# Optimization experiments

Hardware: AMD Instinct MI355X
Metric: run time of the kernel (lower is better)

Reference implementation:

```python
import jax, jax.numpy as jnp
import numpy as np

B, S = 16, 32768
LEVELS = (5, 20)
TIME_DIM = 8
NUM_FREQS = 6  # frequency xyz encoder: 3*(1+2*6)=39 dims
HID = 128
IN_DIM = 3 * (1 + 2 * NUM_FREQS) + 2 * TIME_DIM  # 55


def setup_inputs() -> dict:
    key = jax.random.key(0)
    ks = jax.random.split(key, 16)
    time = jax.random.uniform(ks[0], (B,), dtype=jnp.float32)
    xyz = jax.random.uniform(ks[1], (B, S, 3), dtype=jnp.float32) * 2.0 - 1.0  # in [-1,1]
    te0 = jax.random.normal(ks[2], (LEVELS[0] + 1, TIME_DIM), dtype=jnp.float32)
    te1 = jax.random.normal(ks[3], (LEVELS[1] + 1, TIME_DIM), dtype=jnp.float32)
    W0 = jax.random.normal(ks[4], (IN_DIM, HID), dtype=jnp.float32) * 0.05
    b0 = jnp.zeros((HID,), dtype=jnp.float32)
    W1 = jax.random.normal(ks[5], (HID, HID), dtype=jnp.float32) * 0.05
    b1 = jnp.zeros((HID,), dtype=jnp.float32)
    W2 = jax.random.normal(ks[6], (HID, HID), dtype=jnp.float32) * 0.05
    b2 = jnp.zeros((HID,), dtype=jnp.float32)
    Wout = jax.random.normal(ks[7], (HID, 1), dtype=jnp.float32) * 0.05
    bout = jnp.zeros((1,), dtype=jnp.float32)
    return {"time": time, "xyz": xyz, "te0": te0, "te1": te1,
            "W0": W0, "b0": b0, "W1": W1, "b1": b1, "W2": W2, "b2": b2,
            "Wout": Wout, "bout": bout}


def _time_encode(t, emb, L):
    # bucketize t into L uniform intervals on [0,1), lerp between bucket endpoints
    tL = t * L
    idx = jnp.clip(jnp.floor(tL).astype(jnp.int32), 0, L - 1)  # (B,)
    w = (idx + 1).astype(t.dtype) - tL                          # weight for lower endpoint
    lerped = w[:, None] * emb[idx] + (1.0 - w)[:, None] * emb[idx + 1]
    # t >= 1: use last embedding directly (torch fallback branch)
    return jnp.where((t >= 1.0)[:, None], emb[L][None, :], lerped)


def _xyz_encode(x):
    # frequency encoding, include_input, freqs 2^0..2^(NUM_FREQS-1)
    freqs = jnp.asarray(2.0 ** np.arange(NUM_FREQS), dtype=x.dtype)  # (F,)
    xp = x[:, None, :] * freqs[None, :, None]                         # (N, F, 3)
    n = x.shape[0]
    return jnp.concatenate([x, jnp.sin(xp).reshape(n, -1), jnp.cos(xp).reshape(n, -1)], axis=-1)


def reference(time, xyz, te0, te1, W0, b0, W1, b1, W2, b2, Wout, bout):
    s = xyz.shape[1]
    t_enc = jnp.concatenate([_time_encode(time, te0, LEVELS[0]),
                             _time_encode(time, te1, LEVELS[1])], axis=-1)  # (B, 16)
    t_enc = jnp.repeat(t_enc, s, axis=0)          # (B*S, 16)  'B d -> (B S) d'
    pts = (xyz.reshape(-1, 3) + 1.0) / 2.0        # (B*S, 3)
    x = jnp.concatenate([t_enc, _xyz_encode(pts)], axis=1)  # (B*S, 55)
    x = jax.nn.relu(x @ W0 + b0)
    x = jax.nn.relu(x @ W1 + b1)
    x = jax.nn.relu(x @ W2 + b2)
    return x @ Wout + bout  # (B*S, 1)
```

## Files before the change

kernel.cpp:

```cpp
#include <hip/hip_runtime.h>

typedef _Float16 f16;
typedef __attribute__((ext_vector_type(2))) __fp16 fp16x2;
typedef __attribute__((ext_vector_type(8))) _Float16 f16x8;
typedef __attribute__((ext_vector_type(4))) float f32x4;
typedef __attribute__((ext_vector_type(4))) unsigned int u32x4;

#define NPTS   (16 * 32768)
#define W0P_OFF 0
#define W1P_OFF (16 * 1024)
#define W2P_OFF (48 * 1024)
#define WOP_OFF (80 * 1024)
#define FRAGS_BYTES (84 * 1024)
#define TENC_OFF FRAGS_BYTES
#define WS_NEEDED (FRAGS_BYTES + 1024)
#define LDS_TOTAL (4 * 4096)

__global__ void pack_weights(const float* __restrict__ time, const float* __restrict__ te0,
                             const float* __restrict__ te1, const float* __restrict__ W0,
                             const float* __restrict__ W1, const float* __restrict__ W2,
                             const float* __restrict__ Wout, unsigned char* __restrict__ ws) {
  const int bi = blockIdx.x;
  const int l = threadIdx.x;
  const int g = l >> 4, r16 = l & 15;
  if (bi < 84) {
    const float* W; int obase, fi, kt, mt, kmax; bool natural, outcol;
    if (bi < 16)      { W = W0;   fi = bi;      mt = fi >> 1; kt = fi & 1; obase = W0P_OFF; kmax = 55;  natural = true;  outcol = false; }
    else if (bi < 48) { W = W1;   fi = bi - 16; mt = fi >> 2; kt = fi & 3; obase = W1P_OFF; kmax = 128; natural = false; outcol = false; }
    else if (bi < 80) { W = W2;   fi = bi - 48; mt = fi >> 2; kt = fi & 3; obase = W2P_OFF; kmax = 128; natural = false; outcol = false; }
    else              { W = Wout; fi = bi - 80; mt = 0;       kt = fi;     obase = WOP_OFF; kmax = 128; natural = false; outcol = true;  }
    const int m = mt * 16 + r16;
    f16 vals[8] __attribute__((aligned(16)));
#pragma unroll
    for (int j = 0; j < 8; ++j) {
      const int k = natural ? (kt * 32 + g * 8 + j)
                            : (kt * 32 + (j >> 2) * 16 + g * 4 + (j & 3));
      float v = 0.f;
      if (k < kmax) v = outcol ? ((m == 0) ? Wout[k] : 0.f) : W[k * 128 + m];
      vals[j] = (f16)v;
    }
    *(u32x4*)(ws + obase + (fi * 64 + l) * 16) = *(const u32x4*)vals;
  } else {
    const int idx = (bi - 84) * 64 + l;
    const int b = idx >> 4, d = idx & 15;
    const float t = time[b];
    const float* emb; int L, dd;
    if (d < 8) { emb = te0; L = 5;  dd = d; }
    else       { emb = te1; L = 20; dd = d - 8; }
    const float tL = t * (float)L;
    int i = (int)floorf(tL);
    i = i < 0 ? 0 : (i > L - 1 ? L - 1 : i);
    const float wlo = (float)(i + 1) - tL;
    float v = wlo * emb[i * 8 + dd] + (1.f - wlo) * emb[(i + 1) * 8 + dd];
    if (t >= 1.f) v = emb[L * 8 + dd];
    ((float*)(ws + TENC_OFF))[idx] = v;
  }
}

template <int KT>
__device__ __forceinline__ void layer_swapped(const unsigned char* __restrict__ wsrc,
                                              const float* __restrict__ bias,
                                              const f16x8 (&Bin)[KT][4], f16x8 (&Bout)[4][4],
                                              int lane) {
  const int g4 = (lane >> 4) * 4;
  f16x8 A0b[3], A1b[3];
  f32x4 bv[4][2];
#pragma unroll
  for (int mtp = 0; mtp < 4; ++mtp) {
    bv[mtp][0] = *(const f32x4*)(bias + mtp * 32 + g4);
    bv[mtp][1] = *(const f32x4*)(bias + mtp * 32 + 16 + g4);
  }
#pragma unroll
  for (int s = 0; s < 2; ++s) {
    const int mtp = s / KT, kt = s % KT;
    A0b[s] = *(const f16x8*)(wsrc + (((2 * mtp)     * KT + kt) * 64 + lane) * 16);
    A1b[s] = *(const f16x8*)(wsrc + (((2 * mtp + 1) * KT + kt) * 64 + lane) * 16);
  }
  f32x4 acc[2][2][4];
#pragma unroll
  for (int mtp = 0; mtp < 4; ++mtp) {
    const int par = mtp & 1;
#pragma unroll
    for (int kt = 0; kt < KT; ++kt) {
      const int s = mtp * KT + kt, cb = s % 3;
      if (s + 2 < 4 * KT) {
        const int mtp2 = (s + 2) / KT, kt2 = (s + 2) % KT, pb = (s + 2) % 3;
        A0b[pb] = *(const f16x8*)(wsrc + (((2 * mtp2)     * KT + kt2) * 64 + lane) * 16);
        A1b[pb] = *(const f16x8*)(wsrc + (((2 * mtp2 + 1) * KT + kt2) * 64 + lane) * 16);
      }
      __builtin_amdgcn_s_setprio(1);
      if (kt == 0) {
#pragma unroll
        for (int nt = 0; nt < 4; ++nt)
          acc[par][0][nt] = __builtin_amdgcn_mfma_f32_16x16x32_f16(A0b[cb], Bin[0][nt], bv[mtp][0], 0, 0, 0);
#pragma unroll
        for (int nt = 0; nt < 4; ++nt)
          acc[par][1][nt] = __builtin_amdgcn_mfma_f32_16x16x32_f16(A1b[cb], Bin[0][nt], bv[mtp][1], 0, 0, 0);
      } else {
#pragma unroll
        for (int nt = 0; nt < 4; ++nt)
          acc[par][0][nt] = __builtin_amdgcn_mfma_f32_16x16x32_f16(A0b[cb], Bin[kt][nt], acc[par][0][nt], 0, 0, 0);
#pragma unroll
        for (int nt = 0; nt < 4; ++nt)
          acc[par][1][nt] = __builtin_amdgcn_mfma_f32_16x16x32_f16(A1b[cb], Bin[kt][nt], acc[par][1][nt], 0, 0, 0);
      }
      __builtin_amdgcn_s_setprio(0);
    }
#pragma unroll
    for (int nt = 0; nt < 4; ++nt) {
      union { fp16x2 h2[4]; f16x8 v; } u;
      u.h2[0] = __builtin_amdgcn_cvt_pkrtz(fmaxf(acc[par][0][nt][0], 0.f), fmaxf(acc[par][0][nt][1], 0.f));
      u.h2[1] = __builtin_amdgcn_cvt_pkrtz(fmaxf(acc[par][0][nt][2], 0.f), fmaxf(acc[par][0][nt][3], 0.f));
      u.h2[2] = __builtin_amdgcn_cvt_pkrtz(fmaxf(acc[par][1][nt][0], 0.f), fmaxf(acc[par][1][nt][1], 0.f));
      u.h2[3] = __builtin_amdgcn_cvt_pkrtz(fmaxf(acc[par][1][nt][2], 0.f), fmaxf(acc[par][1][nt][3], 0.f));
      Bout[mtp][nt] = u.v;
    }
  }
}

__global__ void __launch_bounds__(256, 2)
mlp_main(const float* __restrict__ xyz, const float* __restrict__ b0,
         const float* __restrict__ b1, const float* __restrict__ b2,
         const float* __restrict__ bout, const unsigned char* __restrict__ ws,
         float* __restrict__ out) {
  extern __shared__ char lds[];
  const int tid = threadIdx.x;
  const int lane = tid & 63, wv = tid >> 6;
  const int g = lane >> 4, r16 = lane & 15;

  char* scr = lds + wv * 4096;
  const float bo = bout[0];

  const int pbase = blockIdx.x * 256 + wv * 64;
  const int p = pbase + lane;

  float ff[64];
  const float* tb = (const float*)(ws + TENC_OFF) + (blockIdx.x >> 7) * 16;
#pragma unroll
  for (int i = 0; i < 16; ++i) ff[i] = tb[i];
  const float xs0 = xyz[p * 3], xs1 = xyz[p * 3 + 1], xs2 = xyz[p * 3 + 2];
  const float pcs[3] = {(xs0 + 1.f) * 0.5f, (xs1 + 1.f) * 0.5f, (xs2 + 1.f) * 0.5f};
#pragma unroll
  for (int c = 0; c < 3; ++c) {
    ff[16 + c] = pcs[c];
    float s = __sinf(pcs[c]), co = __cosf(pcs[c]);
#pragma unroll
    for (int f = 0; f < 6; ++f) {
      ff[19 + f * 3 + c] = s;
      ff[37 + f * 3 + c] = co;
      const float s2 = 2.f * s * co, c2 = 1.f - 2.f * s * s;
      s = s2; co = c2;
    }
  }
#pragma unroll
  for (int i = 55; i < 64; ++i) ff[i] = 0.f;
  unsigned int fw[32];
#pragma unroll
  for (int i = 0; i < 32; ++i) {
    union { fp16x2 h; unsigned int u; } cv;
    cv.h = __builtin_amdgcn_cvt_pkrtz(ff[2 * i], ff[2 * i + 1]);
    fw[i] = cv.u;
  }

  f16x8 B0[2][4];
#pragma unroll
  for (int h = 0; h < 2; ++h) {
    if ((lane >> 5) == h) {
#pragma unroll
      for (int s = 0; s < 8; ++s)
        *(u32x4*)(scr + (lane & 31) * 128 + ((s ^ (lane & 7)) * 16)) = ((const u32x4*)fw)[s];
    }
    asm volatile("s_waitcnt lgkmcnt(0)" ::: "memory");
#pragma unroll
    for (int kt = 0; kt < 2; ++kt)
#pragma unroll
      for (int nn = 0; nn < 2; ++nn) {
        const int row = nn * 16 + r16;
        B0[kt][h * 2 + nn] = *(const f16x8*)(scr + row * 128 + (((4 * kt + g) ^ (row & 7)) * 16));
      }
    asm volatile("s_waitcnt lgkmcnt(0)" ::: "memory");
  }

  f16x8 Bx[4][4], By[4][4];
  layer_swapped<2>(ws + W0P_OFF, b0, B0, Bx, lane);
  layer_swapped<4>(ws + W1P_OFF, b1, Bx, By, lane);
  layer_swapped<4>(ws + W2P_OFF, b2, By, Bx, lane);

  f16x8 Ab[4];
#pragma unroll
  for (int kt = 0; kt < 4; ++kt)
    Ab[kt] = *(const f16x8*)(ws + WOP_OFF + (kt * 64 + lane) * 16);
  const f32x4 bovec = (f32x4){bo, bo, bo, bo};
  f32x4 accO[4];
  __builtin_amdgcn_s_setprio(1);
#pragma unroll
  for (int nt = 0; nt < 4; ++nt)
    accO[nt] = __builtin_amdgcn_mfma_f32_16x16x32_f16(Ab[0], Bx[0][nt], bovec, 0, 0, 0);
#pragma unroll
  for (int kt = 1; kt < 4; ++kt) {
#pragma unroll
    for (int nt = 0; nt < 4; ++nt)
      accO[nt] = __builtin_amdgcn_mfma_f32_16x16x32_f16(Ab[kt], Bx[kt][nt], accO[nt], 0, 0, 0);
  }
  __builtin_amdgcn_s_setprio(0);

  const float a0 = __shfl(accO[0][0], r16, 64);
  const float a1 = __shfl(accO[1][0], r16, 64);
  const float a2 = __shfl(accO[2][0], r16, 64);
  const float a3 = __shfl(accO[3][0], r16, 64);
  const float v = g == 0 ? a0 : g == 1 ? a1 : g == 2 ? a2 : a3;
  out[pbase + lane] = v;
}

extern "C" void kernel_launch(void* const* d_in, const int* in_sizes, int n_in,
                              void* d_out, int out_size, void* d_ws, size_t ws_size,
                              hipStream_t stream) {
  const float* time = (const float*)d_in[0];
  const float* xyz  = (const float*)d_in[1];
  const float* te0  = (const float*)d_in[2];
  const float* te1  = (const float*)d_in[3];
  const float* W0   = (const float*)d_in[4];
  const float* b0   = (const float*)d_in[5];
  const float* W1   = (const float*)d_in[6];
  const float* b1   = (const float*)d_in[7];
  const float* W2   = (const float*)d_in[8];
  const float* b2   = (const float*)d_in[9];
  const float* Wout = (const float*)d_in[10];
  const float* bout = (const float*)d_in[11];
  float* out = (float*)d_out;
  unsigned char* ws = (unsigned char*)d_ws;
  if (ws_size < WS_NEEDED) return;

  pack_weights<<<88, 64, 0, stream>>>(time, te0, te1, W0, W1, W2, Wout, ws);
  mlp_main<<<NPTS / 256, 256, LDS_TOTAL, stream>>>(xyz, b0, b1, b2, bout, ws, out);
}
```

Measured before the change: 49.79 us.

## Deepen weight-fragment prefetch with manual vmcnt pipelining and stage biases in LDS

Weight fragment loads become inline-asm global loads in a 6-slot ring with a prefetch distance of 5 steps. Explicit s_waitcnt vmcnt counts and sched_barriers gate each MFMA step so loads stay in flight longer. Biases are staged once per block into LDS and read from there at the first k-step of each output tile, replacing the per-layer global bias loads. The accumulator set is halved by flattening the loop and emitting each tile's relu/convert as it completes. The risks are that the hand-counted waits must exactly match the outstanding loads, and that the extra live registers could reduce occupancy.

```diff
diff --git a/kernel.cpp b/kernel.cpp
--- a/kernel.cpp
+++ b/kernel.cpp
@@ -14,7 +14,8 @@
 #define FRAGS_BYTES (84 * 1024)
 #define TENC_OFF FRAGS_BYTES
 #define WS_NEEDED (FRAGS_BYTES + 1024)
-#define LDS_TOTAL (4 * 4096)
+#define BIAS_LDS_OFF (4 * 4096)
+#define LDS_TOTAL (BIAS_LDS_OFF + 1536)
 
 __global__ void pack_weights(const float* __restrict__ time, const float* __restrict__ te0,
                              const float* __restrict__ te1, const float* __restrict__ W0,
@@ -57,63 +58,76 @@
   }
 }
 
+__device__ __forceinline__ u32x4 gload16(const unsigned char* p) {
+  u32x4 r;
+  asm volatile("global_load_dwordx4 %0, %1, off" : "=v"(r) : "v"(p));
+  return r;
+}
+__device__ __forceinline__ f16x8 asf16(u32x4 v) {
+  union { u32x4 u; f16x8 h; } c; c.u = v; return c.h;
+}
+
 template <int KT>
 __device__ __forceinline__ void layer_swapped(const unsigned char* __restrict__ wsrc,
-                                              const float* __restrict__ bias,
+                                              const float* __restrict__ bias_lds,
                                               const f16x8 (&Bin)[KT][4], f16x8 (&Bout)[4][4],
                                               int lane) {
+  constexpr int S = 4 * KT;
   const int g4 = (lane >> 4) * 4;
-  f16x8 A0b[3], A1b[3];
-  f32x4 bv[4][2];
-#pragma unroll
-  for (int mtp = 0; mtp < 4; ++mtp) {
-    bv[mtp][0] = *(const f32x4*)(bias + mtp * 32 + g4);
-    bv[mtp][1] = *(const f32x4*)(bias + mtp * 32 + 16 + g4);
-  }
-#pragma unroll
-  for (int s = 0; s < 2; ++s) {
+  u32x4 A0b[6], A1b[6];
+#pragma unroll
+  for (int s = 0; s < 5; ++s) {
     const int mtp = s / KT, kt = s % KT;
-    A0b[s] = *(const f16x8*)(wsrc + (((2 * mtp)     * KT + kt) * 64 + lane) * 16);
-    A1b[s] = *(const f16x8*)(wsrc + (((2 * mtp + 1) * KT + kt) * 64 + lane) * 16);
-  }
-  f32x4 acc[2][2][4];
-#pragma unroll
-  for (int mtp = 0; mtp < 4; ++mtp) {
-    const int par = mtp & 1;
-#pragma unroll
-    for (int kt = 0; kt < KT; ++kt) {
-      const int s = mtp * KT + kt, cb = s % 3;
-      if (s + 2 < 4 * KT) {
-        const int mtp2 = (s + 2) / KT, kt2 = (s + 2) % KT, pb = (s + 2) % 3;
-        A0b[pb] = *(const f16x8*)(wsrc + (((2 * mtp2)     * KT + kt2) * 64 + lane) * 16);
-        A1b[pb] = *(const f16x8*)(wsrc + (((2 * mtp2 + 1) * KT + kt2) * 64 + lane) * 16);
+    A0b[s] = gload16(wsrc + (((2 * mtp) * KT + kt) * 64 + lane) * 16);
+    A1b[s] = gload16(wsrc + (((2 * mtp + 1) * KT + kt) * 64 + lane) * 16);
+  }
+  f32x4 acc[2][4];
+#pragma unroll
+  for (int s = 0; s < S; ++s) {
+    const int mtp = s / KT, kt = s % KT, cb = s % 6;
+    f32x4 bv0, bv1;
+    if (kt == 0) {
+      bv0 = *(const f32x4*)(bias_lds + mtp * 32 + g4);
+      bv1 = *(const f32x4*)(bias_lds + mtp * 32 + 16 + g4);
+    }
+    if (s + 5 <= S)      asm volatile("s_waitcnt vmcnt(8)");
+    else if (s == S - 4) asm volatile("s_waitcnt vmcnt(6)");
+    else if (s == S - 3) asm volatile("s_waitcnt vmcnt(4)");
+    else if (s == S - 2) asm volatile("s_waitcnt vmcnt(2)");
+    else                 asm volatile("s_waitcnt vmcnt(0)");
+    __builtin_amdgcn_sched_barrier(0);
+    if (s + 5 < S) {
+      const int s2 = s + 5, mtp2 = s2 / KT, kt2 = s2 % KT, pb = s2 % 6;
+      A0b[pb] = gload16(wsrc + (((2 * mtp2) * KT + kt2) * 64 + lane) * 16);
+      A1b[pb] = gload16(wsrc + (((2 * mtp2 + 1) * KT + kt2) * 64 + lane) * 16);
+    }
+    __builtin_amdgcn_s_setprio(1);
+    if (kt == 0) {
+#pragma unroll
+      for (int nt = 0; nt < 4; ++nt)
+        acc[0][nt] = __builtin_amdgcn_mfma_f32_16x16x32_f16(asf16(A0b[cb]), Bin[0][nt], bv0, 0, 0, 0);
+#pragma unroll
+      for (int nt = 0; nt < 4; ++nt)
+        acc[1][nt] = __builtin_amdgcn_mfma_f32_16x16x32_f16(asf16(A1b[cb]), Bin[0][nt], bv1, 0, 0, 0);
+    } else {
+#pragma unroll
+      for (int nt = 0; nt < 4; ++nt)
+        acc[0][nt] = __builtin_amdgcn_mfma_f32_16x16x32_f16(asf16(A0b[cb]), Bin[kt][nt], acc[0][nt], 0, 0, 0);
+#pragma unroll
+      for (int nt = 0; nt < 4; ++nt)
+        acc[1][nt] = __builtin_amdgcn_mfma_f32_16x16x32_f16(asf16(A1b[cb]), Bin[kt][nt], acc[1][nt], 0, 0, 0);
+    }
+    __builtin_amdgcn_s_setprio(0);
+    if (kt == KT - 1) {
+#pragma unroll
+      for (int nt = 0; nt < 4; ++nt) {
+        union { fp16x2 h2[4]; f16x8 v; } u;
+        u.h2[0] = __builtin_amdgcn_cvt_pkrtz(fmaxf(acc[0][nt][0], 0.f), fmaxf(acc[0][nt][1], 0.f));
+        u.h2[1] = __builtin_amdgcn_cvt_pkrtz(fmaxf(acc[0][nt][2], 0.f), fmaxf(acc[0][nt][3], 0.f));
+        u.h2[2] = __builtin_amdgcn_cvt_pkrtz(fmaxf(acc[1][nt][0], 0.f), fmaxf(acc[1][nt][1], 0.f));
+        u.h2[3] = __builtin_amdgcn_cvt_pkrtz(fmaxf(acc[1][nt][2], 0.f), fmaxf(acc[1][nt][3], 0.f));
+        Bout[mtp][nt] = u.v;
       }
-      __builtin_amdgcn_s_setprio(1);
-      if (kt == 0) {
-#pragma unroll
-        for (int nt = 0; nt < 4; ++nt)
-          acc[par][0][nt] = __builtin_amdgcn_mfma_f32_16x16x32_f16(A0b[cb], Bin[0][nt], bv[mtp][0], 0, 0, 0);
-#pragma unroll
-        for (int nt = 0; nt < 4; ++nt)
-          acc[par][1][nt] = __builtin_amdgcn_mfma_f32_16x16x32_f16(A1b[cb], Bin[0][nt], bv[mtp][1], 0, 0, 0);
-      } else {
-#pragma unroll
-        for (int nt = 0; nt < 4; ++nt)
-          acc[par][0][nt] = __builtin_amdgcn_mfma_f32_16x16x32_f16(A0b[cb], Bin[kt][nt], acc[par][0][nt], 0, 0, 0);
-#pragma unroll
-        for (int nt = 0; nt < 4; ++nt)
-          acc[par][1][nt] = __builtin_amdgcn_mfma_f32_16x16x32_f16(A1b[cb], Bin[kt][nt], acc[par][1][nt], 0, 0, 0);
-      }
-      __builtin_amdgcn_s_setprio(0);
-    }
-#pragma unroll
-    for (int nt = 0; nt < 4; ++nt) {
-      union { fp16x2 h2[4]; f16x8 v; } u;
-      u.h2[0] = __builtin_amdgcn_cvt_pkrtz(fmaxf(acc[par][0][nt][0], 0.f), fmaxf(acc[par][0][nt][1], 0.f));
-      u.h2[1] = __builtin_amdgcn_cvt_pkrtz(fmaxf(acc[par][0][nt][2], 0.f), fmaxf(acc[par][0][nt][3], 0.f));
-      u.h2[2] = __builtin_amdgcn_cvt_pkrtz(fmaxf(acc[par][1][nt][0], 0.f), fmaxf(acc[par][1][nt][1], 0.f));
-      u.h2[3] = __builtin_amdgcn_cvt_pkrtz(fmaxf(acc[par][1][nt][2], 0.f), fmaxf(acc[par][1][nt][3], 0.f));
-      Bout[mtp][nt] = u.v;
     }
   }
 }
@@ -128,8 +142,18 @@
   const int lane = tid & 63, wv = tid >> 6;
   const int g = lane >> 4, r16 = lane & 15;
 
+  if (tid < 96) {
+    const int layer = tid >> 5, t = tid & 31;
+    const float* src = layer == 0 ? b0 : (layer == 1 ? b1 : b2);
+    *(float4*)(lds + BIAS_LDS_OFF + layer * 512 + t * 16) = *(const float4*)(src + t * 4);
+  }
+  const float bo = bout[0];
+  __syncthreads();
+
   char* scr = lds + wv * 4096;
-  const float bo = bout[0];
+  const float* bl0 = (const float*)(lds + BIAS_LDS_OFF);
+  const float* bl1 = (const float*)(lds + BIAS_LDS_OFF + 512);
+  const float* bl2 = (const float*)(lds + BIAS_LDS_OFF + 1024);
 
   const int pbase = blockIdx.x * 256 + wv * 64;
   const int p = pbase + lane;
@@ -181,26 +205,30 @@
     asm volatile("s_waitcnt lgkmcnt(0)" ::: "memory");
   }
 
+  asm volatile("s_waitcnt vmcnt(0)");
+
   f16x8 Bx[4][4], By[4][4];
-  layer_swapped<2>(ws + W0P_OFF, b0, B0, Bx, lane);
-  layer_swapped<4>(ws + W1P_OFF, b1, Bx, By, lane);
-  layer_swapped<4>(ws + W2P_OFF, b2, By, Bx, lane);
-
-  f16x8 Ab[4];
+  layer_swapped<2>(ws + W0P_OFF, bl0, B0, Bx, lane);
+  layer_swapped<4>(ws + W1P_OFF, bl1, Bx, By, lane);
+  layer_swapped<4>(ws + W2P_OFF, bl2, By, Bx, lane);
+
+  u32x4 Ob[4];
 #pragma unroll
   for (int kt = 0; kt < 4; ++kt)
-    Ab[kt] = *(const f16x8*)(ws + WOP_OFF + (kt * 64 + lane) * 16);
+    Ob[kt] = gload16(ws + WOP_OFF + (kt * 64 + lane) * 16);
+  asm volatile("s_waitcnt vmcnt(0)");
+  __builtin_amdgcn_sched_barrier(0);
   const f32x4 bovec = (f32x4){bo, bo, bo, bo};
   f32x4 accO[4];
   __builtin_amdgcn_s_setprio(1);
 #pragma unroll
   for (int nt = 0; nt < 4; ++nt)
-    accO[nt] = __builtin_amdgcn_mfma_f32_16x16x32_f16(Ab[0], Bx[0][nt], bovec, 0, 0, 0);
+    accO[nt] = __builtin_amdgcn_mfma_f32_16x16x32_f16(asf16(Ob[0]), Bx[0][nt], bovec, 0, 0, 0);
 #pragma unroll
   for (int kt = 1; kt < 4; ++kt) {
 #pragma unroll
     for (int nt = 0; nt < 4; ++nt)
-      accO[nt] = __builtin_amdgcn_mfma_f32_16x16x32_f16(Ab[kt], Bx[kt][nt], accO[nt], 0, 0, 0);
+      accO[nt] = __builtin_amdgcn_mfma_f32_16x16x32_f16(asf16(Ob[kt]), Bx[kt][nt], accO[nt], 0, 0, 0);
   }
   __builtin_amdgcn_s_setprio(0);
 
```

After: 50.81 us. +2.0%, slower.

## Use single-wave blocks, streamline layer accumulators, and fuse ReLU into packed f16 max

Applied to the files above, without the earlier changes.

Switches the main kernel from 256-thread, 4-wave blocks to 64-thread single-wave blocks with their own 4 KB LDS scratch, raising the block count and giving finer-grained scheduling. The layer routine drops the double-buffered accumulators and preloaded bias array, loading the bias only at the start of each output tile, which reduces register pressure. ReLU is now applied after fp16 packing with v_pk_max_f16 instead of per-element fmaxf in fp32. The occupancy hint becomes (64,4), which may cap waves per SIMD differently than before.

```diff
diff --git a/kernel.cpp b/kernel.cpp
--- a/kernel.cpp
+++ b/kernel.cpp
@@ -14,7 +14,7 @@
 #define FRAGS_BYTES (84 * 1024)
 #define TENC_OFF FRAGS_BYTES
 #define WS_NEEDED (FRAGS_BYTES + 1024)
-#define LDS_TOTAL (4 * 4096)
+#define LDS_TOTAL 4096
 
 __global__ void pack_weights(const float* __restrict__ time, const float* __restrict__ te0,
                              const float* __restrict__ te1, const float* __restrict__ W0,
@@ -57,6 +57,17 @@
   }
 }
 
+__device__ __forceinline__ unsigned int pkmax0(unsigned int x) {
+  unsigned int r;
+  asm("v_pk_max_f16 %0, %1, %2" : "=v"(r) : "v"(x), "v"(0u));
+  return r;
+}
+__device__ __forceinline__ unsigned int pkrtz(float a, float b) {
+  union { fp16x2 h; unsigned int u; } c;
+  c.h = __builtin_amdgcn_cvt_pkrtz(a, b);
+  return c.u;
+}
+
 template <int KT>
 __device__ __forceinline__ void layer_swapped(const unsigned char* __restrict__ wsrc,
                                               const float* __restrict__ bias,
@@ -64,78 +75,70 @@
                                               int lane) {
   const int g4 = (lane >> 4) * 4;
   f16x8 A0b[3], A1b[3];
-  f32x4 bv[4][2];
-#pragma unroll
-  for (int mtp = 0; mtp < 4; ++mtp) {
-    bv[mtp][0] = *(const f32x4*)(bias + mtp * 32 + g4);
-    bv[mtp][1] = *(const f32x4*)(bias + mtp * 32 + 16 + g4);
-  }
+  float4 ba, bb;
+  f32x4 acc[2][4];
 #pragma unroll
   for (int s = 0; s < 2; ++s) {
     const int mtp = s / KT, kt = s % KT;
     A0b[s] = *(const f16x8*)(wsrc + (((2 * mtp)     * KT + kt) * 64 + lane) * 16);
     A1b[s] = *(const f16x8*)(wsrc + (((2 * mtp + 1) * KT + kt) * 64 + lane) * 16);
   }
-  f32x4 acc[2][2][4];
-#pragma unroll
-  for (int mtp = 0; mtp < 4; ++mtp) {
-    const int par = mtp & 1;
-#pragma unroll
-    for (int kt = 0; kt < KT; ++kt) {
-      const int s = mtp * KT + kt, cb = s % 3;
-      if (s + 2 < 4 * KT) {
-        const int mtp2 = (s + 2) / KT, kt2 = (s + 2) % KT, pb = (s + 2) % 3;
-        A0b[pb] = *(const f16x8*)(wsrc + (((2 * mtp2)     * KT + kt2) * 64 + lane) * 16);
-        A1b[pb] = *(const f16x8*)(wsrc + (((2 * mtp2 + 1) * KT + kt2) * 64 + lane) * 16);
+#pragma unroll
+  for (int s = 0; s < 4 * KT; ++s) {
+    const int mtp = s / KT, kt = s % KT, cb = s % 3;
+    if (kt == 0) {
+      ba = *(const float4*)(bias + mtp * 32 + g4);
+      bb = *(const float4*)(bias + mtp * 32 + 16 + g4);
+#pragma unroll
+      for (int nt = 0; nt < 4; ++nt) {
+        acc[0][nt] = (f32x4){ba.x, ba.y, ba.z, ba.w};
+        acc[1][nt] = (f32x4){bb.x, bb.y, bb.z, bb.w};
       }
-      __builtin_amdgcn_s_setprio(1);
-      if (kt == 0) {
-#pragma unroll
-        for (int nt = 0; nt < 4; ++nt)
-          acc[par][0][nt] = __builtin_amdgcn_mfma_f32_16x16x32_f16(A0b[cb], Bin[0][nt], bv[mtp][0], 0, 0, 0);
-#pragma unroll
-        for (int nt = 0; nt < 4; ++nt)
-          acc[par][1][nt] = __builtin_amdgcn_mfma_f32_16x16x32_f16(A1b[cb], Bin[0][nt], bv[mtp][1], 0, 0, 0);
-      } else {
-#pragma unroll
-        for (int nt = 0; nt < 4; ++nt)
-          acc[par][0][nt] = __builtin_amdgcn_mfma_f32_16x16x32_f16(A0b[cb], Bin[kt][nt], acc[par][0][nt], 0, 0, 0);
-#pragma unroll
-        for (int nt = 0; nt < 4; ++nt)
-          acc[par][1][nt] = __builtin_amdgcn_mfma_f32_16x16x32_f16(A1b[cb], Bin[kt][nt], acc[par][1][nt], 0, 0, 0);
+    }
+    if (s + 2 < 4 * KT) {
+      const int mtp2 = (s + 2) / KT, kt2 = (s + 2) % KT, pb = (s + 2) % 3;
+      A0b[pb] = *(const f16x8*)(wsrc + (((2 * mtp2)     * KT + kt2) * 64 + lane) * 16);
+      A1b[pb] = *(const f16x8*)(wsrc + (((2 * mtp2 + 1) * KT + kt2) * 64 + lane) * 16);
+    }
+    __builtin_amdgcn_s_setprio(1);
+#pragma unroll
+    for (int nt = 0; nt < 4; ++nt)
+      acc[0][nt] = __builtin_amdgcn_mfma_f32_16x16x32_f16(A0b[cb], Bin[kt][nt], acc[0][nt], 0, 0, 0);
+#pragma unroll
+    for (int nt = 0; nt < 4; ++nt)
+      acc[1][nt] = __builtin_amdgcn_mfma_f32_16x16x32_f16(A1b[cb], Bin[kt][nt], acc[1][nt], 0, 0, 0);
+    __builtin_amdgcn_s_setprio(0);
+    if (kt == KT - 1) {
+#pragma unroll
+      for (int nt = 0; nt < 4; ++nt) {
+        union { unsigned int w[4]; f16x8 v; } u;
+        u.w[0] = pkmax0(pkrtz(acc[0][nt][0], acc[0][nt][1]));
+        u.w[1] = pkmax0(pkrtz(acc[0][nt][2], acc[0][nt][3]));
+        u.w[2] = pkmax0(pkrtz(acc[1][nt][0], acc[1][nt][1]));
+        u.w[3] = pkmax0(pkrtz(acc[1][nt][2], acc[1][nt][3]));
+        Bout[mtp][nt] = u.v;
       }
-      __builtin_amdgcn_s_setprio(0);
-    }
-#pragma unroll
-    for (int nt = 0; nt < 4; ++nt) {
-      union { fp16x2 h2[4]; f16x8 v; } u;
-      u.h2[0] = __builtin_amdgcn_cvt_pkrtz(fmaxf(acc[par][0][nt][0], 0.f), fmaxf(acc[par][0][nt][1], 0.f));
-      u.h2[1] = __builtin_amdgcn_cvt_pkrtz(fmaxf(acc[par][0][nt][2], 0.f), fmaxf(acc[par][0][nt][3], 0.f));
-      u.h2[2] = __builtin_amdgcn_cvt_pkrtz(fmaxf(acc[par][1][nt][0], 0.f), fmaxf(acc[par][1][nt][1], 0.f));
-      u.h2[3] = __builtin_amdgcn_cvt_pkrtz(fmaxf(acc[par][1][nt][2], 0.f), fmaxf(acc[par][1][nt][3], 0.f));
-      Bout[mtp][nt] = u.v;
-    }
-  }
-}
-
-__global__ void __launch_bounds__(256, 2)
+    }
+  }
+}
+
+__global__ void __launch_bounds__(64, 4)
 mlp_main(const float* __restrict__ xyz, const float* __restrict__ b0,
          const float* __restrict__ b1, const float* __restrict__ b2,
          const float* __restrict__ bout, const unsigned char* __restrict__ ws,
          float* __restrict__ out) {
   extern __shared__ char lds[];
-  const int tid = threadIdx.x;
-  const int lane = tid & 63, wv = tid >> 6;
+  const int lane = threadIdx.x;
   const int g = lane >> 4, r16 = lane & 15;
 
-  char* scr = lds + wv * 4096;
+  char* scr = lds;
   const float bo = bout[0];
 
-  const int pbase = blockIdx.x * 256 + wv * 64;
+  const int pbase = blockIdx.x * 64;
   const int p = pbase + lane;
 
   float ff[64];
-  const float* tb = (const float*)(ws + TENC_OFF) + (blockIdx.x >> 7) * 16;
+  const float* tb = (const float*)(ws + TENC_OFF) + (blockIdx.x >> 9) * 16;
 #pragma unroll
   for (int i = 0; i < 16; ++i) ff[i] = tb[i];
   const float xs0 = xyz[p * 3], xs1 = xyz[p * 3 + 1], xs2 = xyz[p * 3 + 2];
@@ -156,11 +159,7 @@
   for (int i = 55; i < 64; ++i) ff[i] = 0.f;
   unsigned int fw[32];
 #pragma unroll
-  for (int i = 0; i < 32; ++i) {
-    union { fp16x2 h; unsigned int u; } cv;
-    cv.h = __builtin_amdgcn_cvt_pkrtz(ff[2 * i], ff[2 * i + 1]);
-    fw[i] = cv.u;
-  }
+  for (int i = 0; i < 32; ++i) fw[i] = pkrtz(ff[2 * i], ff[2 * i + 1]);
 
   f16x8 B0[2][4];
 #pragma unroll
@@ -232,5 +231,5 @@
   if (ws_size < WS_NEEDED) return;
 
   pack_weights<<<88, 64, 0, stream>>>(time, te0, te1, W0, W1, W2, Wout, ws);
-  mlp_main<<<NPTS / 256, 256, LDS_TOTAL, stream>>>(xyz, b0, b1, b2, bout, ws, out);
-}
+  mlp_main<<<NPTS / 64, 64, LDS_TOTAL, stream>>>(xyz, b0, b1, b2, bout, ws, out);
+}
```

After: 111.0 us. 123% more time.
